# Optimization experiments

Hardware: AMD Instinct MI355X
Metric: run time of the kernel (lower is better)

The kernel has to match this reference:

```python
import jax, jax.numpy as jnp
import numpy as np

SIGMA = 1.0


def setup_inputs() -> dict:
    key = jax.random.key(0)
    z = jax.random.normal(key, (8192, 128), dtype=jnp.float32)
    return {"z": z}


def reference(z) -> jnp.ndarray:
    # Pairwise squared L2 distance via the GEMM identity:
    #   ||zi - zj||^2 = ||zi||^2 + ||zj||^2 - 2 zi . zj
    # Same math as broadcast-subtract-square-sum, without the [N,N,D] intermediate.
    sq = jnp.sum(z * z, axis=-1)                      # [N]
    gram = z @ z.T                                    # [N, N]
    d2 = sq[:, None] + sq[None, :] - 2.0 * gram       # [N, N]
    d2 = jnp.maximum(d2, 0.0)  # clamp tiny negatives from cancellation
    return jnp.exp(-d2 / SIGMA)
```

## Files before the change

### kernel.cpp

```cpp
#include <hip/hip_runtime.h>
#include <hip/hip_bf16.h>

#define N 8192
#define Dd 128

typedef short short8 __attribute__((ext_vector_type(8)));
typedef float floatx4 __attribute__((ext_vector_type(4)));

static __device__ inline unsigned short f2bf(float f) {
    unsigned int u = __float_as_uint(f);
    unsigned int r = (u + 0x7fffu + ((u >> 16) & 1u)) >> 16;
    return (unsigned short)r;
}
static __device__ inline float bf2f(unsigned short b) {
    return __uint_as_float(((unsigned int)b) << 16);
}

__global__ __launch_bounds__(256) void prep_kernel(const float* __restrict__ z,
                                                   unsigned short* __restrict__ zb,
                                                   float* __restrict__ sq) {
    int row  = blockIdx.x * 4 + (threadIdx.x >> 6);
    int lane = threadIdx.x & 63;
    float2 v = ((const float2*)z)[row * 64 + lane];
    unsigned short b0 = f2bf(v.x);
    unsigned short b1 = f2bf(v.y);
    float f0 = bf2f(b0), f1 = bf2f(b1);
    ushort2 st; st.x = b0; st.y = b1;
    ((ushort2*)zb)[row * 64 + lane] = st;
    float s = f0 * f0 + f1 * f1;
    #pragma unroll
    for (int off = 32; off > 0; off >>= 1) s += __shfl_down(s, off, 64);
    if (lane == 0) sq[row] = s;
}

__global__ __launch_bounds__(256, 2) void pairsim_kernel(const unsigned short* __restrict__ zb,
                                                         const float* __restrict__ sq,
                                                         float* __restrict__ out) {
    __shared__ unsigned short lA[128 * 128];
    __shared__ unsigned short lB[128 * 128];

    int bx = blockIdx.x, by = blockIdx.y;
    int colBase = bx * 128, rowBase = by * 128;
    int t  = threadIdx.x;
    int r0 = t >> 4, cg = t & 15;

    const uint4* gA = (const uint4*)(zb + (size_t)rowBase * Dd);
    const uint4* gB = (const uint4*)(zb + (size_t)colBase * Dd);
    uint4 va[8], vb[8];
    #pragma unroll
    for (int i = 0; i < 8; i++) va[i] = gA[(r0 + i * 16) * 16 + cg];
    #pragma unroll
    for (int i = 0; i < 8; i++) vb[i] = gB[(r0 + i * 16) * 16 + cg];

    int scg = ((cg ^ r0) * 8);
    #pragma unroll
    for (int i = 0; i < 8; i++) *(uint4*)&lA[(r0 + i * 16) * 128 + scg] = va[i];
    #pragma unroll
    for (int i = 0; i < 8; i++) *(uint4*)&lB[(r0 + i * 16) * 128 + scg] = vb[i];
    __syncthreads();

    int w = t >> 6, lane = t & 63;
    int wr = (w >> 1) * 64, wc = (w & 1) * 64;
    int m = lane & 15, quad = lane >> 4;

    floatx4 zero = {0.f, 0.f, 0.f, 0.f};
    floatx4 acc[4][4];
    #pragma unroll
    for (int i = 0; i < 4; i++)
        #pragma unroll
        for (int j = 0; j < 4; j++) acc[i][j] = zero;

    #pragma unroll
    for (int ks = 0; ks < 4; ks++) {
        short8 af[4], bfr[4];
        int c = ks * 4 + quad;
        #pragma unroll
        for (int i = 0; i < 4; i++)
            af[i] = *(const short8*)&lA[(wr + i * 16 + m) * 128 + ((c ^ m) * 8)];
        #pragma unroll
        for (int j = 0; j < 4; j++)
            bfr[j] = *(const short8*)&lB[(wc + j * 16 + m) * 128 + ((c ^ m) * 8)];
        #pragma unroll
        for (int i = 0; i < 4; i++)
            #pragma unroll
            for (int j = 0; j < 4; j++)
                acc[i][j] = __builtin_amdgcn_mfma_f32_16x16x32_bf16(af[i], bfr[j], acc[i][j], 0, 0, 0);
    }

    #pragma unroll
    for (int j = 0; j < 4; j++) {
        int col = colBase + wc + j * 16 + m;
        float sc = sq[col];
        #pragma unroll
        for (int i = 0; i < 4; i++) {
            #pragma unroll
            for (int r = 0; r < 4; r++) {
                int row = rowBase + wr + i * 16 + quad * 4 + r;
                float sr = sq[row];
                float g = acc[i][j][r];
                float e = fminf(2.0f * g - sr - sc, 0.0f);
                out[(size_t)row * N + col] = __expf(e);
            }
        }
    }
}

extern "C" void kernel_launch(void* const* d_in, const int* in_sizes, int n_in,
                              void* d_out, int out_size, void* d_ws, size_t ws_size,
                              hipStream_t stream) {
    const float* z = (const float*)d_in[0];
    unsigned short* zb = (unsigned short*)d_ws;
    float* sqv = (float*)((char*)d_ws + (size_t)N * Dd * sizeof(unsigned short));
    float* out = (float*)d_out;

    prep_kernel<<<N / 4, 256, 0, stream>>>(z, zb, sqv);
    pairsim_kernel<<<dim3(64, 64), 256, 0, stream>>>(zb, sqv, out);
}
```

Before: 263.3 us.

## Fuse bf16 conversion and row norms into pairsim kernel, use nontemporal stores

Removes the separate prep kernel. Each tile block now loads fp32 z directly, converts it to bf16 into LDS, and computes squared norms with a 16-lane shuffle reduction into shared arrays. Output writes switch to nontemporal stores to avoid polluting cache with the 256MB output. This saves one launch and the workspace round trip, but every block redoes the conversion and reads twice as many input bytes.

```diff
diff --git a/kernel.cpp b/kernel.cpp
--- a/kernel.cpp
+++ b/kernel.cpp
@@ -9,54 +9,75 @@
 
 static __device__ inline unsigned short f2bf(float f) {
     unsigned int u = __float_as_uint(f);
-    unsigned int r = (u + 0x7fffu + ((u >> 16) & 1u)) >> 16;
-    return (unsigned short)r;
+    return (unsigned short)((u + 0x7fffu + ((u >> 16) & 1u)) >> 16);
 }
 static __device__ inline float bf2f(unsigned short b) {
     return __uint_as_float(((unsigned int)b) << 16);
 }
 
-__global__ __launch_bounds__(256) void prep_kernel(const float* __restrict__ z,
-                                                   unsigned short* __restrict__ zb,
-                                                   float* __restrict__ sq) {
-    int row  = blockIdx.x * 4 + (threadIdx.x >> 6);
-    int lane = threadIdx.x & 63;
-    float2 v = ((const float2*)z)[row * 64 + lane];
-    unsigned short b0 = f2bf(v.x);
-    unsigned short b1 = f2bf(v.y);
-    float f0 = bf2f(b0), f1 = bf2f(b1);
-    ushort2 st; st.x = b0; st.y = b1;
-    ((ushort2*)zb)[row * 64 + lane] = st;
-    float s = f0 * f0 + f1 * f1;
-    #pragma unroll
-    for (int off = 32; off > 0; off >>= 1) s += __shfl_down(s, off, 64);
-    if (lane == 0) sq[row] = s;
-}
-
-__global__ __launch_bounds__(256, 2) void pairsim_kernel(const unsigned short* __restrict__ zb,
-                                                         const float* __restrict__ sq,
+__global__ __launch_bounds__(256, 2) void pairsim_kernel(const float* __restrict__ z,
                                                          float* __restrict__ out) {
     __shared__ unsigned short lA[128 * 128];
     __shared__ unsigned short lB[128 * 128];
+    __shared__ float sqA[128], sqB[128];
 
     int bx = blockIdx.x, by = blockIdx.y;
     int colBase = bx * 128, rowBase = by * 128;
     int t  = threadIdx.x;
     int r0 = t >> 4, cg = t & 15;
 
-    const uint4* gA = (const uint4*)(zb + (size_t)rowBase * Dd);
-    const uint4* gB = (const uint4*)(zb + (size_t)colBase * Dd);
-    uint4 va[8], vb[8];
+    const float4* gA = (const float4*)(z + (size_t)rowBase * Dd);
+    const float4* gB = (const float4*)(z + (size_t)colBase * Dd);
+
+    float sA[8], sB[8];
     #pragma unroll
-    for (int i = 0; i < 8; i++) va[i] = gA[(r0 + i * 16) * 16 + cg];
+    for (int i = 0; i < 8; i++) {
+        int row = r0 + i * 16;
+        float4 a0 = gA[row * 32 + 2 * cg];
+        float4 a1 = gA[row * 32 + 2 * cg + 1];
+        float fs[8] = {a0.x, a0.y, a0.z, a0.w, a1.x, a1.y, a1.z, a1.w};
+        float s = 0.f;
+        short8 pk;
+        #pragma unroll
+        for (int e = 0; e < 8; e++) {
+            unsigned short h = f2bf(fs[e]);
+            float fr = bf2f(h);
+            s += fr * fr;
+            pk[e] = (short)h;
+        }
+        *(short8*)&lA[row * 128 + ((cg ^ r0) * 8)] = pk;
+        sA[i] = s;
+    }
     #pragma unroll
-    for (int i = 0; i < 8; i++) vb[i] = gB[(r0 + i * 16) * 16 + cg];
+    for (int i = 0; i < 8; i++) {
+        int row = r0 + i * 16;
+        float4 b0 = gB[row * 32 + 2 * cg];
+        float4 b1 = gB[row * 32 + 2 * cg + 1];
+        float fs[8] = {b0.x, b0.y, b0.z, b0.w, b1.x, b1.y, b1.z, b1.w};
+        float s = 0.f;
+        short8 pk;
+        #pragma unroll
+        for (int e = 0; e < 8; e++) {
+            unsigned short h = f2bf(fs[e]);
+            float fr = bf2f(h);
+            s += fr * fr;
+            pk[e] = (short)h;
+        }
+        *(short8*)&lB[row * 128 + ((cg ^ r0) * 8)] = pk;
+        sB[i] = s;
+    }
 
-    int scg = ((cg ^ r0) * 8);
     #pragma unroll
-    for (int i = 0; i < 8; i++) *(uint4*)&lA[(r0 + i * 16) * 128 + scg] = va[i];
-    #pragma unroll
-    for (int i = 0; i < 8; i++) *(uint4*)&lB[(r0 + i * 16) * 128 + scg] = vb[i];
+    for (int i = 0; i < 8; i++) {
+        float s = sA[i];
+        #pragma unroll
+        for (int off = 8; off > 0; off >>= 1) s += __shfl_down(s, off, 16);
+        if (cg == 0) sqA[r0 + i * 16] = s;
+        float sb = sB[i];
+        #pragma unroll
+        for (int off = 8; off > 0; off >>= 1) sb += __shfl_down(sb, off, 16);
+        if (cg == 0) sqB[r0 + i * 16] = sb;
+    }
     __syncthreads();
 
     int w = t >> 6, lane = t & 63;
@@ -89,17 +110,18 @@
 
     #pragma unroll
     for (int j = 0; j < 4; j++) {
-        int col = colBase + wc + j * 16 + m;
-        float sc = sq[col];
+        int cl = wc + j * 16 + m;
+        float sc = sqB[cl];
         #pragma unroll
         for (int i = 0; i < 4; i++) {
             #pragma unroll
             for (int r = 0; r < 4; r++) {
-                int row = rowBase + wr + i * 16 + quad * 4 + r;
-                float sr = sq[row];
+                int rl = wr + i * 16 + quad * 4 + r;
+                float sr = sqA[rl];
                 float g = acc[i][j][r];
                 float e = fminf(2.0f * g - sr - sc, 0.0f);
-                out[(size_t)row * N + col] = __expf(e);
+                __builtin_nontemporal_store(__expf(e),
+                    &out[(size_t)(rowBase + rl) * N + colBase + cl]);
             }
         }
     }
@@ -109,10 +131,6 @@
                               void* d_out, int out_size, void* d_ws, size_t ws_size,
                               hipStream_t stream) {
     const float* z = (const float*)d_in[0];
-    unsigned short* zb = (unsigned short*)d_ws;
-    float* sqv = (float*)((char*)d_ws + (size_t)N * Dd * sizeof(unsigned short));
     float* out = (float*)d_out;
-
-    prep_kernel<<<N / 4, 256, 0, stream>>>(z, zb, sqv);
-    pairsim_kernel<<<dim3(64, 64), 256, 0, stream>>>(zb, sqv, out);
+    pairsim_kernel<<<dim3(64, 64), 256, 0, stream>>>(z, out);
 }
```

Measured after the change: 297.0 us. 1.13x slower.
